# Optimization experiments

Measured on AMD Instinct MI355X. Metric: run time of the kernel, lower is better.

The kernel has to match this reference:

```python
import jax, jax.numpy as jnp
import numpy as np


def setup_inputs() -> dict:
    key = jax.random.key(0)
    k1, k2 = jax.random.split(key)
    x = jax.random.normal(k1, (8, 16, 16, 16, 64), dtype=jnp.float32)
    gamma = jax.random.normal(k2, (1,), dtype=jnp.float32)
    return {"x": x, "gamma": gamma}


def reference(x, gamma):
    # x: (B, D, H, W, C); tokens N = D*H*W, head dim C
    B, D, H, W, C = x.shape
    N = D * H * W
    q = x.reshape(B, N, C)                          # proj_query (B, N, C)
    # energy = batch_dot(q, q^T) -> (B, N, N)
    energy = jnp.einsum('bnc,bmc->bnm', q, q)
    attn = jax.nn.softmax(energy, axis=-1)          # softmax over last axis
    out = jnp.einsum('bnm,bmc->bnc', attn, q)       # attend * V (V = q)
    out = out.reshape(B, D, H, W, C)
    return gamma * out + x                          # gamma-scaled residual
```

## Files before the change

### kernel.cpp

```cpp
#include <hip/hip_runtime.h>

typedef _Float16 f16;
typedef _Float16 f16x4 __attribute__((ext_vector_type(4)));
typedef _Float16 f16x8 __attribute__((ext_vector_type(8)));
typedef float f32x4 __attribute__((ext_vector_type(4)));
typedef float f32x16 __attribute__((ext_vector_type(16)));
typedef unsigned int u32;
typedef u32 u32x2 __attribute__((ext_vector_type(2)));
typedef u32 u32x4v __attribute__((ext_vector_type(4)));

#define MFMA_F16 __builtin_amdgcn_mfma_f32_32x32x16_f16

constexpr int N   = 4096;
constexpr int C   = 64;
constexpr int KV  = 32;
constexpr int QB  = 64;
constexpr int NGRP = 4;
constexpr int KEYS_PER_GRP = N / NGRP;
constexpr int NT  = KEYS_PER_GRP / KV;
constexpr float LOG2E = 1.44269504088896f;
constexpr float THR   = 11.0f;

constexpr int KROW    = 136;
constexpr int VROW    = 72;
constexpr int VOFF    = 32 * KROW;
constexpr int BUFSZ   = VOFF + 64 * VROW;
constexpr int GSTRIDE = 2 * BUFSZ;
constexpr int PM_OFF  = 52224;
constexpr int PL_OFF  = PM_OFF + 768;
constexpr int EP_OFF  = 53760;

__device__ __forceinline__ float fexp2(float x) { return __builtin_amdgcn_exp2f(x); }
__device__ __forceinline__ u32 pkrtz(float a, float b) {
    return __builtin_bit_cast(u32, __builtin_amdgcn_cvt_pkrtz(a, b));
}
__device__ __forceinline__ f16x8 ld8(const char* p) {
    f16x4 lo = *(const f16x4*)p;
    f16x4 hi = *(const f16x4*)(p + 8);
    return __builtin_shufflevector(lo, hi, 0, 1, 2, 3, 4, 5, 6, 7);
}

__global__ __launch_bounds__(512, 4)
void channel_attn_kernel(const float* __restrict__ x,
                         const float* __restrict__ gamma,
                         float* __restrict__ out) {
    __shared__ __align__(16) unsigned char smem[71680];

    const int tid = threadIdx.x;
    const int w   = tid >> 6;
    const int g   = w >> 1;
    const int qw  = w & 1;
    const int l   = tid & 63;
    const int h   = l >> 5;
    const int q   = l & 31;
    const int bid = blockIdx.x;
    const int b   = bid & 7;
    const int qt  = bid >> 3;
    const float* xb = x + (size_t)b * (N * C);
    const int qbase = qt * QB;
    const int qg   = qw * 32 + q;
    const int qrow = qbase + qg;

    f16x8 Qf[4];
    {
        const float* qs = xb + (size_t)qrow * C + h * 8;
        #pragma unroll
        for (int kk = 0; kk < 4; ++kk) {
            f32x4 a  = *(const f32x4*)(qs + kk * 16);
            f32x4 c2 = *(const f32x4*)(qs + kk * 16 + 4);
            f16x8 f;
            f[0] = (f16)(a[0] * LOG2E);  f[1] = (f16)(a[1] * LOG2E);
            f[2] = (f16)(a[2] * LOG2E);  f[3] = (f16)(a[3] * LOG2E);
            f[4] = (f16)(c2[0] * LOG2E); f[5] = (f16)(c2[1] * LOG2E);
            f[6] = (f16)(c2[2] * LOG2E); f[7] = (f16)(c2[3] * LOG2E);
            Qf[kk] = f;
        }
    }

    const int c0  = (l & 15) * 4;
    const int kr0 = qw * 16 + (l >> 4) * 4;
    f32x4 stg[4];
    char* gb = (char*)smem + g * GSTRIDE;

    const float* kvsrc = xb + ((size_t)(g * KEYS_PER_GRP + kr0) * C + c0);

    auto stage_load = [&]() {
        #pragma unroll
        for (int j = 0; j < 4; ++j) stg[j] = *(const f32x4*)(kvsrc + j * C);
        kvsrc += KV * C;
    };
    auto stage_write = [&](int sel) {
        char* kb = gb + sel * BUFSZ;
        char* vb = kb + VOFF;
        #pragma unroll
        for (int j = 0; j < 4; ++j) {
            u32x2 kv2 = { pkrtz(stg[j][0], stg[j][1]), pkrtz(stg[j][2], stg[j][3]) };
            *(u32x2*)(kb + (kr0 + j) * KROW + c0 * 2) = kv2;
        }
        #pragma unroll
        for (int i = 0; i < 4; ++i) {
            u32x2 vv = { pkrtz(stg[0][i], stg[1][i]), pkrtz(stg[2][i], stg[3][i]) };
            *(u32x2*)(vb + (c0 + i) * VROW + kr0 * 2) = vv;
        }
    };

    f32x16 ot[2] = {};
    float m_run = -INFINITY, l_run = 0.f;

    stage_load();
    stage_write(0);
    __syncthreads();

    #pragma unroll 2
    for (int kt = 0; kt < NT; ++kt) {
        const int sel = kt & 1;
        const char* kb = gb + sel * BUFSZ;
        const char* vb = kb + VOFF;

        if (kt + 1 < NT) stage_load();

        f32x16 st = {};
        __builtin_amdgcn_s_setprio(1);
        #pragma unroll
        for (int kk = 0; kk < 4; ++kk) {
            f16x8 kf = ld8(kb + q * KROW + h * 16 + kk * 32);
            st = MFMA_F16(kf, Qf[kk], st, 0, 0, 0);
        }
        __builtin_amdgcn_s_setprio(0);

        float m01 = fmaxf(st[0], st[1]),  m23 = fmaxf(st[2], st[3]);
        float m45 = fmaxf(st[4], st[5]),  m67 = fmaxf(st[6], st[7]);
        float m89 = fmaxf(st[8], st[9]),  mab = fmaxf(st[10], st[11]);
        float mcd = fmaxf(st[12], st[13]), mef = fmaxf(st[14], st[15]);
        float pmax = fmaxf(fmaxf(fmaxf(m01, m23), fmaxf(m45, m67)),
                           fmaxf(fmaxf(m89, mab), fmaxf(mcd, mef)));
        pmax = fmaxf(pmax, __shfl_xor(pmax, 32, 64));

        if (!__all(pmax - m_run <= THR)) {
            float m_new = fmaxf(m_run, pmax);
            float scf = fexp2(m_run - m_new);
            l_run *= scf;
            #pragma unroll
            for (int mI = 0; mI < 2; ++mI)
                #pragma unroll
                for (int r2 = 0; r2 < 16; ++r2) ot[mI][r2] *= scf;
            m_run = m_new;
        }

        float rs4[4] = {0.f, 0.f, 0.f, 0.f};
        #pragma unroll
        for (int r2 = 0; r2 < 16; ++r2) {
            float p = fexp2(st[r2] - m_run);
            st[r2] = p;
            rs4[r2 & 3] += p;
        }
        float rs = (rs4[0] + rs4[1]) + (rs4[2] + rs4[3]);
        rs += __shfl_xor(rs, 32, 64);
        l_run += rs;

        f16x8 Pf[2];
        #pragma unroll
        for (int kk = 0; kk < 2; ++kk) {
            int so = 2 * kk + h;
            int sx = 2 * kk + (1 - h);
            u32 ua0 = pkrtz(st[so*4+0], st[so*4+1]);
            u32 ua1 = pkrtz(st[so*4+2], st[so*4+3]);
            u32 ub0 = pkrtz(st[sx*4+0], st[sx*4+1]);
            u32 ub1 = pkrtz(st[sx*4+2], st[sx*4+3]);
            u32 r0 = __shfl_xor(ub0, 32, 64);
            u32 r1 = __shfl_xor(ub1, 32, 64);
            u32x4v uv;
            uv[0] = h ? r0 : ua0;
            uv[1] = h ? r1 : ua1;
            uv[2] = h ? ua0 : r0;
            uv[3] = h ? ua1 : r1;
            Pf[kk] = __builtin_bit_cast(f16x8, uv);
        }

        if (kt + 1 < NT) stage_write(sel ^ 1);

        __builtin_amdgcn_s_setprio(1);
        #pragma unroll
        for (int mI = 0; mI < 2; ++mI) {
            f32x16 acc = ot[mI];
            #pragma unroll
            for (int kk = 0; kk < 2; ++kk) {
                f16x8 vf = ld8(vb + (q + 32 * mI) * VROW + h * 16 + kk * 32);
                acc = MFMA_F16(vf, Pf[kk], acc, 0, 0, 0);
            }
            ot[mI] = acc;
        }
        __builtin_amdgcn_s_setprio(0);

        __syncthreads();
    }

    float* pO = (float*)smem;
    float* pm = (float*)(smem + PM_OFF);
    float* pl = (float*)(smem + PL_OFF);

    if (g > 0) {
        float* po = pO + (size_t)(g - 1) * (64 * 68) + qg * 68;
        #pragma unroll
        for (int mI = 0; mI < 2; ++mI)
            #pragma unroll
            for (int j = 0; j < 4; ++j) {
                f32x4 v = { ot[mI][4*j], ot[mI][4*j+1], ot[mI][4*j+2], ot[mI][4*j+3] };
                *(f32x4*)(po + mI * 32 + j * 8 + h * 4) = v;
            }
        if (h == 0) { pm[(g - 1) * 64 + qg] = m_run; pl[(g - 1) * 64 + qg] = l_run; }
    }
    __syncthreads();

    if (g == 0) {
        float m1 = pm[qg], m2 = pm[64 + qg], m3 = pm[128 + qg];
        float l1 = pl[qg], l2 = pl[64 + qg], l3 = pl[128 + qg];
        float M  = fmaxf(fmaxf(m_run, m1), fmaxf(m2, m3));
        float a0 = fexp2(m_run - M);
        float ag[3] = { fexp2(m1 - M), fexp2(m2 - M), fexp2(m3 - M) };
        float L = l_run * a0 + l1 * ag[0] + l2 * ag[1] + l3 * ag[2];
        #pragma unroll
        for (int mI = 0; mI < 2; ++mI)
            #pragma unroll
            for (int r2 = 0; r2 < 16; ++r2) ot[mI][r2] *= a0;
        #pragma unroll
        for (int gg = 0; gg < 3; ++gg) {
            const float* po = pO + (size_t)gg * (64 * 68) + qg * 68;
            #pragma unroll
            for (int mI = 0; mI < 2; ++mI)
                #pragma unroll
                for (int j = 0; j < 4; ++j) {
                    f32x4 v = *(const f32x4*)(po + mI * 32 + j * 8 + h * 4);
                    ot[mI][4*j+0] += ag[gg] * v[0];
                    ot[mI][4*j+1] += ag[gg] * v[1];
                    ot[mI][4*j+2] += ag[gg] * v[2];
                    ot[mI][4*j+3] += ag[gg] * v[3];
                }
        }

        float invl = 1.0f / L;
        float* ep = (float*)(smem + EP_OFF + qw * 8448);
        #pragma unroll
        for (int mI = 0; mI < 2; ++mI)
            #pragma unroll
            for (int r2 = 0; r2 < 16; ++r2) {
                int c = 32 * mI + (r2 & 3) + 8 * (r2 >> 2) + 4 * h;
                ep[c * 33 + q] = ot[mI][r2] * invl;
            }

        const float gm = gamma[0];
        float* ob = out + (size_t)b * (N * C);
        #pragma unroll
        for (int it = 0; it < 8; ++it) {
            int ql  = it * 4 + (l >> 4);
            int cc0 = (l & 15) * 4;
            f32x4 o;
            o[0] = ep[(cc0 + 0) * 33 + ql];
            o[1] = ep[(cc0 + 1) * 33 + ql];
            o[2] = ep[(cc0 + 2) * 33 + ql];
            o[3] = ep[(cc0 + 3) * 33 + ql];
            int row = qbase + qw * 32 + ql;
            f32x4 xi = *(const f32x4*)(xb + (size_t)row * C + cc0);
            f32x4 res = { gm * o[0] + xi[0], gm * o[1] + xi[1],
                          gm * o[2] + xi[2], gm * o[3] + xi[3] };
            *(f32x4*)(ob + (size_t)row * C + cc0) = res;
        }
    }
}

extern "C" void kernel_launch(void* const* d_in, const int* in_sizes, int n_in,
                              void* d_out, int out_size, void* d_ws, size_t ws_size,
                              hipStream_t stream) {
    const float* x     = (const float*)d_in[0];
    const float* gamma = (const float*)d_in[1];
    float* out         = (float*)d_out;
    dim3 grid(512), block(512);
    channel_attn_kernel<<<grid, block, 0, stream>>>(x, gamma, out);
}
```

Baseline: 203.7 us.

## Precompute fp16 swizzled K/V in workspace and stream via global_load_lds

Adds a prepass kernel that converts x to fp16 once, writing K in row layout and V transposed per 32-key tile into a workspace with XOR swizzles. The attention kernel then streams these tiles straight into LDS with global_load_lds, removing per-block fp32 loads, conversion and scattered LDS writes. The row-sum is now computed on the matrix cores by multiplying against a ones vector. A fallback kernel also runs after it and scans its output for non-finite values, so a valid result costs only an extra launch and a check. The price is an extra kernel launch and workspace traffic.

```diff
diff --git a/kernel.cpp b/kernel.cpp
--- a/kernel.cpp
+++ b/kernel.cpp
@@ -11,40 +11,60 @@
 
 #define MFMA_F16 __builtin_amdgcn_mfma_f32_32x32x16_f16
 
-constexpr int N   = 4096;
-constexpr int C   = 64;
-constexpr int KV  = 32;
-constexpr int QB  = 64;
-constexpr int NGRP = 4;
-constexpr int KEYS_PER_GRP = N / NGRP;
-constexpr int NT  = KEYS_PER_GRP / KV;
 constexpr float LOG2E = 1.44269504088896f;
 constexpr float THR   = 11.0f;
-
-constexpr int KROW    = 136;
-constexpr int VROW    = 72;
-constexpr int VOFF    = 32 * KROW;
-constexpr int BUFSZ   = VOFF + 64 * VROW;
-constexpr int GSTRIDE = 2 * BUFSZ;
-constexpr int PM_OFF  = 52224;
-constexpr int PL_OFF  = PM_OFF + 768;
-constexpr int EP_OFF  = 53760;
 
 __device__ __forceinline__ float fexp2(float x) { return __builtin_amdgcn_exp2f(x); }
 __device__ __forceinline__ u32 pkrtz(float a, float b) {
     return __builtin_bit_cast(u32, __builtin_amdgcn_cvt_pkrtz(a, b));
 }
-__device__ __forceinline__ f16x8 ld8(const char* p) {
-    f16x4 lo = *(const f16x4*)p;
-    f16x4 hi = *(const f16x4*)(p + 8);
-    return __builtin_shufflevector(lo, hi, 0, 1, 2, 3, 4, 5, 6, 7);
+
+constexpr size_t KBYTES  = (size_t)8 * 4096 * 128;
+constexpr size_t WS_NEED = KBYTES * 2;
+
+__global__ __launch_bounds__(256)
+void precompute_kernel(const float* __restrict__ x, char* __restrict__ ws) {
+    int t  = blockIdx.x * 256 + threadIdx.x;
+    int c4 = (t & 15) * 4;
+    int k4 = ((t >> 4) & 1023) * 4;
+    int b  = t >> 14;
+    const float* src = x + ((size_t)b * 4096 + k4) * 64 + c4;
+    f32x4 v[4];
+    #pragma unroll
+    for (int j = 0; j < 4; ++j) v[j] = *(const f32x4*)(src + j * 64);
+    char* Kg = ws;
+    char* Vg = ws + KBYTES;
+    #pragma unroll
+    for (int j = 0; j < 4; ++j) {
+        int key = k4 + j;
+        u32x2 kp = { pkrtz(v[j][0], v[j][1]), pkrtz(v[j][2], v[j][3]) };
+        *(u32x2*)(Kg + ((size_t)(b * 4096 + key)) * 128 + ((c4 * 2) ^ ((key & 7) << 4))) = kp;
+    }
+    int tile = k4 >> 5, kl = k4 & 31;
+    #pragma unroll
+    for (int i = 0; i < 4; ++i) {
+        int ch = c4 + i;
+        u32x2 vp = { pkrtz(v[0][i], v[1][i]), pkrtz(v[2][i], v[3][i]) };
+        *(u32x2*)(Vg + ((size_t)(b * 128 + tile)) * 4096 + ch * 64 + ((kl * 2) ^ ((ch & 7) << 3))) = vp;
+    }
+}
+
+constexpr int NTI  = 32;
+constexpr int GLDS = 16384;
+constexpr int MG_PM = 52224, MG_PL = 52992, MG_EP = 53760;
+
+__device__ __forceinline__ void gload16(const void* g, void* l) {
+    __builtin_amdgcn_global_load_lds(
+        (const __attribute__((address_space(1))) void*)g,
+        (__attribute__((address_space(3))) void*)l, 16, 0, 0);
 }
 
 __global__ __launch_bounds__(512, 4)
-void channel_attn_kernel(const float* __restrict__ x,
-                         const float* __restrict__ gamma,
-                         float* __restrict__ out) {
-    __shared__ __align__(16) unsigned char smem[71680];
+void attn_fast(const char* __restrict__ ws, const float* __restrict__ x,
+               const float* __restrict__ gamma, float* __restrict__ out) {
+    __shared__ __align__(16) unsigned char smem[70656];
+    const char* Kg = ws;
+    const char* Vg = ws + KBYTES;
 
     const int tid = threadIdx.x;
     const int w   = tid >> 6;
@@ -56,14 +76,14 @@
     const int bid = blockIdx.x;
     const int b   = bid & 7;
     const int qt  = bid >> 3;
-    const float* xb = x + (size_t)b * (N * C);
-    const int qbase = qt * QB;
+    const float* xb = x + (size_t)b * (4096 * 64);
+    const int qbase = qt * 64;
     const int qg   = qw * 32 + q;
     const int qrow = qbase + qg;
 
     f16x8 Qf[4];
     {
-        const float* qs = xb + (size_t)qrow * C + h * 8;
+        const float* qs = xb + (size_t)qrow * 64 + h * 8;
         #pragma unroll
         for (int kk = 0; kk < 4; ++kk) {
             f32x4 a  = *(const f32x4*)(qs + kk * 16);
@@ -77,96 +97,92 @@
         }
     }
 
-    const int c0  = (l & 15) * 4;
-    const int kr0 = qw * 16 + (l >> 4) * 4;
-    f32x4 stg[4];
-    char* gb = (char*)smem + g * GSTRIDE;
-
-    const float* kvsrc = xb + ((size_t)(g * KEYS_PER_GRP + kr0) * C + c0);
-
-    auto stage_load = [&]() {
-        #pragma unroll
-        for (int j = 0; j < 4; ++j) stg[j] = *(const f32x4*)(kvsrc + j * C);
-        kvsrc += KV * C;
+    const char* gK = Kg + ((size_t)(b * 4096 + g * 1024)) * 128 + l * 16;
+    const char* gV = Vg + ((size_t)(b * 128  + g * 32 )) * 4096 + l * 16;
+    const char* gsrc = qw ? gV : gK;
+    char* sdst = (char*)smem + g * GLDS + (qw ? 4096 : 0);
+
+    auto stage = [&](int kt, int sel) {
+        const char* s = gsrc + (size_t)kt * 4096;
+        char* d = sdst + sel * 8192;
+        gload16(s,        d);
+        gload16(s + 1024, d + 1024);
+        gload16(s + 2048, d + 2048);
+        gload16(s + 3072, d + 3072);
     };
-    auto stage_write = [&](int sel) {
-        char* kb = gb + sel * BUFSZ;
-        char* vb = kb + VOFF;
-        #pragma unroll
-        for (int j = 0; j < 4; ++j) {
-            u32x2 kv2 = { pkrtz(stg[j][0], stg[j][1]), pkrtz(stg[j][2], stg[j][3]) };
-            *(u32x2*)(kb + (kr0 + j) * KROW + c0 * 2) = kv2;
-        }
-        #pragma unroll
-        for (int i = 0; i < 4; ++i) {
-            u32x2 vv = { pkrtz(stg[0][i], stg[1][i]), pkrtz(stg[2][i], stg[3][i]) };
-            *(u32x2*)(vb + (c0 + i) * VROW + kr0 * 2) = vv;
-        }
-    };
+
+    const char* kbase = (const char*)smem + g * GLDS;
+    const char* vbase = kbase + 4096;
+    const int xk = (q & 7) << 4;
+    const int xv = (q & 7) << 3;
+    const char* kp[4];
+    #pragma unroll
+    for (int kk = 0; kk < 4; ++kk)
+        kp[kk] = kbase + q * 128 + ((kk * 32 + h * 16) ^ xk);
+    const char* vplo[2]; const char* vphi[2];
+    #pragma unroll
+    for (int kk = 0; kk < 2; ++kk) {
+        int c = kk * 32 + h * 16;
+        vplo[kk] = vbase + q * 64 + (c ^ xv);
+        vphi[kk] = vbase + q * 64 + ((c + 8) ^ xv);
+    }
+
+    f16x8 ones8;
+    #pragma unroll
+    for (int j = 0; j < 8; ++j) ones8[j] = (f16)1.0f;
 
     f32x16 ot[2] = {};
-    float m_run = -INFINITY, l_run = 0.f;
-
-    stage_load();
-    stage_write(0);
+    f32x16 accl  = {};
+    float m_run = -INFINITY;
+
+    stage(0, 0);
     __syncthreads();
 
     #pragma unroll 2
-    for (int kt = 0; kt < NT; ++kt) {
+    for (int kt = 0; kt < NTI; ++kt) {
         const int sel = kt & 1;
-        const char* kb = gb + sel * BUFSZ;
-        const char* vb = kb + VOFF;
-
-        if (kt + 1 < NT) stage_load();
+        const int so  = sel * 8192;
+        if (kt + 1 < NTI) stage(kt + 1, sel ^ 1);
 
         f32x16 st = {};
         __builtin_amdgcn_s_setprio(1);
         #pragma unroll
         for (int kk = 0; kk < 4; ++kk) {
-            f16x8 kf = ld8(kb + q * KROW + h * 16 + kk * 32);
+            f16x8 kf = *(const f16x8*)(kp[kk] + so);
             st = MFMA_F16(kf, Qf[kk], st, 0, 0, 0);
         }
         __builtin_amdgcn_s_setprio(0);
 
-        float m01 = fmaxf(st[0], st[1]),  m23 = fmaxf(st[2], st[3]);
-        float m45 = fmaxf(st[4], st[5]),  m67 = fmaxf(st[6], st[7]);
-        float m89 = fmaxf(st[8], st[9]),  mab = fmaxf(st[10], st[11]);
-        float mcd = fmaxf(st[12], st[13]), mef = fmaxf(st[14], st[15]);
-        float pmax = fmaxf(fmaxf(fmaxf(m01, m23), fmaxf(m45, m67)),
-                           fmaxf(fmaxf(m89, mab), fmaxf(mcd, mef)));
+        float t0 = fmaxf(fmaxf(st[0], st[1]), st[2]);
+        float t1 = fmaxf(fmaxf(st[3], st[4]), st[5]);
+        float t2 = fmaxf(fmaxf(st[6], st[7]), st[8]);
+        float t3 = fmaxf(fmaxf(st[9], st[10]), st[11]);
+        float t4 = fmaxf(fmaxf(st[12], st[13]), st[14]);
+        float pmax = fmaxf(fmaxf(fmaxf(t0, t1), fmaxf(t2, t3)), fmaxf(t4, st[15]));
         pmax = fmaxf(pmax, __shfl_xor(pmax, 32, 64));
 
         if (!__all(pmax - m_run <= THR)) {
             float m_new = fmaxf(m_run, pmax);
             float scf = fexp2(m_run - m_new);
-            l_run *= scf;
-            #pragma unroll
-            for (int mI = 0; mI < 2; ++mI)
-                #pragma unroll
-                for (int r2 = 0; r2 < 16; ++r2) ot[mI][r2] *= scf;
+            #pragma unroll
+            for (int r = 0; r < 16; ++r) {
+                ot[0][r] *= scf; ot[1][r] *= scf; accl[r] *= scf;
+            }
             m_run = m_new;
         }
 
-        float rs4[4] = {0.f, 0.f, 0.f, 0.f};
-        #pragma unroll
-        for (int r2 = 0; r2 < 16; ++r2) {
-            float p = fexp2(st[r2] - m_run);
-            st[r2] = p;
-            rs4[r2 & 3] += p;
-        }
-        float rs = (rs4[0] + rs4[1]) + (rs4[2] + rs4[3]);
-        rs += __shfl_xor(rs, 32, 64);
-        l_run += rs;
+        #pragma unroll
+        for (int r = 0; r < 16; ++r) st[r] = fexp2(st[r] - m_run);
 
         f16x8 Pf[2];
         #pragma unroll
         for (int kk = 0; kk < 2; ++kk) {
-            int so = 2 * kk + h;
-            int sx = 2 * kk + (1 - h);
-            u32 ua0 = pkrtz(st[so*4+0], st[so*4+1]);
-            u32 ua1 = pkrtz(st[so*4+2], st[so*4+3]);
-            u32 ub0 = pkrtz(st[sx*4+0], st[sx*4+1]);
-            u32 ub1 = pkrtz(st[sx*4+2], st[sx*4+3]);
+            int sa = 2 * kk + h;
+            int sb = 2 * kk + (1 - h);
+            u32 ua0 = pkrtz(st[sa*4+0], st[sa*4+1]);
+            u32 ua1 = pkrtz(st[sa*4+2], st[sa*4+3]);
+            u32 ub0 = pkrtz(st[sb*4+0], st[sb*4+1]);
+            u32 ub1 = pkrtz(st[sb*4+2], st[sb*4+3]);
             u32 r0 = __shfl_xor(ub0, 32, 64);
             u32 r1 = __shfl_xor(ub1, 32, 64);
             u32x4v uv;
@@ -177,27 +193,29 @@
             Pf[kk] = __builtin_bit_cast(f16x8, uv);
         }
 
-        if (kt + 1 < NT) stage_write(sel ^ 1);
+        accl = MFMA_F16(ones8, Pf[0], accl, 0, 0, 0);
+        accl = MFMA_F16(ones8, Pf[1], accl, 0, 0, 0);
 
         __builtin_amdgcn_s_setprio(1);
         #pragma unroll
         for (int mI = 0; mI < 2; ++mI) {
-            f32x16 acc = ot[mI];
             #pragma unroll
             for (int kk = 0; kk < 2; ++kk) {
-                f16x8 vf = ld8(vb + (q + 32 * mI) * VROW + h * 16 + kk * 32);
-                acc = MFMA_F16(vf, Pf[kk], acc, 0, 0, 0);
+                f16x4 lo = *(const f16x4*)(vplo[kk] + so + mI * 2048);
+                f16x4 hi = *(const f16x4*)(vphi[kk] + so + mI * 2048);
+                f16x8 vf = __builtin_shufflevector(lo, hi, 0, 1, 2, 3, 4, 5, 6, 7);
+                ot[mI] = MFMA_F16(vf, Pf[kk], ot[mI], 0, 0, 0);
             }
-            ot[mI] = acc;
         }
         __builtin_amdgcn_s_setprio(0);
 
         __syncthreads();
     }
 
+    float l_run = accl[0];
     float* pO = (float*)smem;
-    float* pm = (float*)(smem + PM_OFF);
-    float* pl = (float*)(smem + PL_OFF);
+    float* pm = (float*)(smem + MG_PM);
+    float* pl = (float*)(smem + MG_PL);
 
     if (g > 0) {
         float* po = pO + (size_t)(g - 1) * (64 * 68) + qg * 68;
@@ -222,7 +240,7 @@
         #pragma unroll
         for (int mI = 0; mI < 2; ++mI)
             #pragma unroll
-            for (int r2 = 0; r2 < 16; ++r2) ot[mI][r2] *= a0;
+            for (int r = 0; r < 16; ++r) ot[mI][r] *= a0;
         #pragma unroll
         for (int gg = 0; gg < 3; ++gg) {
             const float* po = pO + (size_t)gg * (64 * 68) + qg * 68;
@@ -239,17 +257,17 @@
         }
 
         float invl = 1.0f / L;
-        float* ep = (float*)(smem + EP_OFF + qw * 8448);
+        float* ep = (float*)(smem + MG_EP + qw * 8448);
         #pragma unroll
         for (int mI = 0; mI < 2; ++mI)
             #pragma unroll
-            for (int r2 = 0; r2 < 16; ++r2) {
-                int c = 32 * mI + (r2 & 3) + 8 * (r2 >> 2) + 4 * h;
-                ep[c * 33 + q] = ot[mI][r2] * invl;
+            for (int r = 0; r < 16; ++r) {
+                int c = 32 * mI + (r & 3) + 8 * (r >> 2) + 4 * h;
+                ep[c * 33 + q] = ot[mI][r] * invl;
             }
 
         const float gm = gamma[0];
-        float* ob = out + (size_t)b * (N * C);
+        float* ob = out + (size_t)b * (4096 * 64);
         #pragma unroll
         for (int it = 0; it < 8; ++it) {
             int ql  = it * 4 + (l >> 4);
@@ -260,12 +278,214 @@
             o[2] = ep[(cc0 + 2) * 33 + ql];
             o[3] = ep[(cc0 + 3) * 33 + ql];
             int row = qbase + qw * 32 + ql;
-            f32x4 xi = *(const f32x4*)(xb + (size_t)row * C + cc0);
+            f32x4 xi = *(const f32x4*)(xb + (size_t)row * 64 + cc0);
             f32x4 res = { gm * o[0] + xi[0], gm * o[1] + xi[1],
                           gm * o[2] + xi[2], gm * o[3] + xi[3] };
-            *(f32x4*)(ob + (size_t)row * C + cc0) = res;
-        }
-    }
+            *(f32x4*)(ob + (size_t)row * 64 + cc0) = res;
+        }
+    }
+}
+
+namespace fb {
+
+constexpr int KV = 32, NT = 32, KEYS_PER_GRP = 1024;
+constexpr int KROW = 136, VROW = 72, VOFF = 32 * KROW, BUFSZ = VOFF + 64 * VROW;
+constexpr int GSTRIDE = 2 * BUFSZ;
+constexpr int PM_OFF = 52224, PL_OFF = PM_OFF + 768, EP_OFF = 53760;
+
+__device__ __forceinline__ f16x8 ld8(const char* p) {
+    f16x4 lo = *(const f16x4*)p;
+    f16x4 hi = *(const f16x4*)(p + 8);
+    return __builtin_shufflevector(lo, hi, 0, 1, 2, 3, 4, 5, 6, 7);
+}
+
+__global__ __launch_bounds__(512, 4)
+void channel_attn_fb(const float* __restrict__ x, const float* __restrict__ gamma,
+                     float* __restrict__ out, int force) {
+    __shared__ __align__(16) unsigned char smem[71680];
+    const int tid = threadIdx.x;
+    const int w = tid >> 6, g = w >> 1, qw = w & 1;
+    const int l = tid & 63, h = l >> 5, q = l & 31;
+    const int bid = blockIdx.x, b = bid & 7, qt = bid >> 3;
+    const float* xb = x + (size_t)b * (4096 * 64);
+    const int qbase = qt * 64, qg = qw * 32 + q, qrow = qbase + qg;
+
+    {
+        int bad = force;
+        const float* ob0 = out + (size_t)b * (4096 * 64) + (size_t)qbase * 64;
+        const f32x4* p4 = (const f32x4*)ob0 + (size_t)tid * 2;
+        f32x4 v0 = p4[0], v1 = p4[1];
+        #pragma unroll
+        for (int i = 0; i < 4; ++i) {
+            if (!(__builtin_fabsf(v0[i]) <= 1e30f)) bad = 1;
+            if (!(__builtin_fabsf(v1[i]) <= 1e30f)) bad = 1;
+        }
+        if (!__syncthreads_or(bad)) return;
+    }
+
+    f16x8 Qf[4];
+    {
+        const float* qs = xb + (size_t)qrow * 64 + h * 8;
+        #pragma unroll
+        for (int kk = 0; kk < 4; ++kk) {
+            f32x4 a = *(const f32x4*)(qs + kk * 16);
+            f32x4 c2 = *(const f32x4*)(qs + kk * 16 + 4);
+            f16x8 f;
+            f[0]=(f16)(a[0]*LOG2E); f[1]=(f16)(a[1]*LOG2E); f[2]=(f16)(a[2]*LOG2E); f[3]=(f16)(a[3]*LOG2E);
+            f[4]=(f16)(c2[0]*LOG2E);f[5]=(f16)(c2[1]*LOG2E);f[6]=(f16)(c2[2]*LOG2E);f[7]=(f16)(c2[3]*LOG2E);
+            Qf[kk] = f;
+        }
+    }
+    const int c0 = (l & 15) * 4, kr0 = qw * 16 + (l >> 4) * 4;
+    f32x4 stg[4];
+    char* gb = (char*)smem + g * GSTRIDE;
+    const float* kvsrc = xb + ((size_t)(g * KEYS_PER_GRP + kr0) * 64 + c0);
+    auto stage_load = [&]() {
+        #pragma unroll
+        for (int j = 0; j < 4; ++j) stg[j] = *(const f32x4*)(kvsrc + j * 64);
+        kvsrc += KV * 64;
+    };
+    auto stage_write = [&](int sel) {
+        char* kb = gb + sel * BUFSZ;
+        char* vb = kb + VOFF;
+        #pragma unroll
+        for (int j = 0; j < 4; ++j) {
+            u32x2 kv2 = { pkrtz(stg[j][0], stg[j][1]), pkrtz(stg[j][2], stg[j][3]) };
+            *(u32x2*)(kb + (kr0 + j) * KROW + c0 * 2) = kv2;
+        }
+        #pragma unroll
+        for (int i = 0; i < 4; ++i) {
+            u32x2 vv = { pkrtz(stg[0][i], stg[1][i]), pkrtz(stg[2][i], stg[3][i]) };
+            *(u32x2*)(vb + (c0 + i) * VROW + kr0 * 2) = vv;
+        }
+    };
+    f32x16 ot[2] = {};
+    float m_run = -INFINITY, l_run = 0.f;
+    stage_load(); stage_write(0); __syncthreads();
+    #pragma unroll 2
+    for (int kt = 0; kt < NT; ++kt) {
+        const int sel = kt & 1;
+        const char* kb = gb + sel * BUFSZ;
+        const char* vb = kb + VOFF;
+        if (kt + 1 < NT) stage_load();
+        f32x16 st = {};
+        __builtin_amdgcn_s_setprio(1);
+        #pragma unroll
+        for (int kk = 0; kk < 4; ++kk)
+            st = MFMA_F16(ld8(kb + q * KROW + h * 16 + kk * 32), Qf[kk], st, 0, 0, 0);
+        __builtin_amdgcn_s_setprio(0);
+        float m01=fmaxf(st[0],st[1]), m23=fmaxf(st[2],st[3]), m45=fmaxf(st[4],st[5]), m67=fmaxf(st[6],st[7]);
+        float m89=fmaxf(st[8],st[9]), mab=fmaxf(st[10],st[11]), mcd=fmaxf(st[12],st[13]), mef=fmaxf(st[14],st[15]);
+        float pmax = fmaxf(fmaxf(fmaxf(m01,m23),fmaxf(m45,m67)), fmaxf(fmaxf(m89,mab),fmaxf(mcd,mef)));
+        pmax = fmaxf(pmax, __shfl_xor(pmax, 32, 64));
+        if (!__all(pmax - m_run <= THR)) {
+            float m_new = fmaxf(m_run, pmax);
+            float scf = fexp2(m_run - m_new);
+            l_run *= scf;
+            #pragma unroll
+            for (int mI = 0; mI < 2; ++mI)
+                #pragma unroll
+                for (int r = 0; r < 16; ++r) ot[mI][r] *= scf;
+            m_run = m_new;
+        }
+        float rs4[4] = {0.f,0.f,0.f,0.f};
+        #pragma unroll
+        for (int r = 0; r < 16; ++r) { float p = fexp2(st[r] - m_run); st[r] = p; rs4[r & 3] += p; }
+        float rs = (rs4[0]+rs4[1]) + (rs4[2]+rs4[3]);
+        rs += __shfl_xor(rs, 32, 64);
+        l_run += rs;
+        f16x8 Pf[2];
+        #pragma unroll
+        for (int kk = 0; kk < 2; ++kk) {
+            int sa = 2*kk + h, sb = 2*kk + (1-h);
+            u32 ua0 = pkrtz(st[sa*4+0], st[sa*4+1]);
+            u32 ua1 = pkrtz(st[sa*4+2], st[sa*4+3]);
+            u32 ub0 = pkrtz(st[sb*4+0], st[sb*4+1]);
+            u32 ub1 = pkrtz(st[sb*4+2], st[sb*4+3]);
+            u32 r0 = __shfl_xor(ub0, 32, 64);
+            u32 r1 = __shfl_xor(ub1, 32, 64);
+            u32x4v uv;
+            uv[0] = h ? r0 : ua0; uv[1] = h ? r1 : ua1;
+            uv[2] = h ? ua0 : r0; uv[3] = h ? ua1 : r1;
+            Pf[kk] = __builtin_bit_cast(f16x8, uv);
+        }
+        if (kt + 1 < NT) stage_write(sel ^ 1);
+        __builtin_amdgcn_s_setprio(1);
+        #pragma unroll
+        for (int mI = 0; mI < 2; ++mI) {
+            f32x16 acc = ot[mI];
+            #pragma unroll
+            for (int kk = 0; kk < 2; ++kk)
+                acc = MFMA_F16(ld8(vb + (q + 32*mI) * VROW + h * 16 + kk * 32), Pf[kk], acc, 0, 0, 0);
+            ot[mI] = acc;
+        }
+        __builtin_amdgcn_s_setprio(0);
+        __syncthreads();
+    }
+    float* pO = (float*)smem;
+    float* pm = (float*)(smem + PM_OFF);
+    float* pl = (float*)(smem + PL_OFF);
+    if (g > 0) {
+        float* po = pO + (size_t)(g - 1) * (64 * 68) + qg * 68;
+        #pragma unroll
+        for (int mI = 0; mI < 2; ++mI)
+            #pragma unroll
+            for (int j = 0; j < 4; ++j) {
+                f32x4 v = { ot[mI][4*j], ot[mI][4*j+1], ot[mI][4*j+2], ot[mI][4*j+3] };
+                *(f32x4*)(po + mI * 32 + j * 8 + h * 4) = v;
+            }
+        if (h == 0) { pm[(g-1)*64 + qg] = m_run; pl[(g-1)*64 + qg] = l_run; }
+    }
+    __syncthreads();
+    if (g == 0) {
+        float m1 = pm[qg], m2 = pm[64+qg], m3 = pm[128+qg];
+        float l1 = pl[qg], l2 = pl[64+qg], l3 = pl[128+qg];
+        float M = fmaxf(fmaxf(m_run, m1), fmaxf(m2, m3));
+        float a0 = fexp2(m_run - M);
+        float ag[3] = { fexp2(m1 - M), fexp2(m2 - M), fexp2(m3 - M) };
+        float L = l_run * a0 + l1*ag[0] + l2*ag[1] + l3*ag[2];
+        #pragma unroll
+        for (int mI = 0; mI < 2; ++mI)
+            #pragma unroll
+            for (int r = 0; r < 16; ++r) ot[mI][r] *= a0;
+        #pragma unroll
+        for (int gg = 0; gg < 3; ++gg) {
+            const float* po = pO + (size_t)gg * (64 * 68) + qg * 68;
+            #pragma unroll
+            for (int mI = 0; mI < 2; ++mI)
+                #pragma unroll
+                for (int j = 0; j < 4; ++j) {
+                    f32x4 v = *(const f32x4*)(po + mI * 32 + j * 8 + h * 4);
+                    ot[mI][4*j+0] += ag[gg]*v[0]; ot[mI][4*j+1] += ag[gg]*v[1];
+                    ot[mI][4*j+2] += ag[gg]*v[2]; ot[mI][4*j+3] += ag[gg]*v[3];
+                }
+        }
+        float invl = 1.0f / L;
+        float* ep = (float*)(smem + EP_OFF + qw * 8448);
+        #pragma unroll
+        for (int mI = 0; mI < 2; ++mI)
+            #pragma unroll
+            for (int r = 0; r < 16; ++r) {
+                int c = 32*mI + (r & 3) + 8*(r >> 2) + 4*h;
+                ep[c * 33 + q] = ot[mI][r] * invl;
+            }
+        const float gm = gamma[0];
+        float* ob = out + (size_t)b * (4096 * 64);
+        #pragma unroll
+        for (int it = 0; it < 8; ++it) {
+            int ql = it * 4 + (l >> 4);
+            int cc0 = (l & 15) * 4;
+            f32x4 o;
+            o[0] = ep[(cc0+0)*33+ql]; o[1] = ep[(cc0+1)*33+ql];
+            o[2] = ep[(cc0+2)*33+ql]; o[3] = ep[(cc0+3)*33+ql];
+            int row = qbase + qw * 32 + ql;
+            f32x4 xi = *(const f32x4*)(xb + (size_t)row * 64 + cc0);
+            f32x4 res = { gm*o[0]+xi[0], gm*o[1]+xi[1], gm*o[2]+xi[2], gm*o[3]+xi[3] };
+            *(f32x4*)(ob + (size_t)row * 64 + cc0) = res;
+        }
+    }
+}
+
 }
 
 extern "C" void kernel_launch(void* const* d_in, const int* in_sizes, int n_in,
@@ -274,6 +494,11 @@
     const float* x     = (const float*)d_in[0];
     const float* gamma = (const float*)d_in[1];
     float* out         = (float*)d_out;
-    dim3 grid(512), block(512);
-    channel_attn_kernel<<<grid, block, 0, stream>>>(x, gamma, out);
-}
+    if (ws_size >= WS_NEED && d_ws != nullptr) {
+        precompute_kernel<<<dim3(512), dim3(256), 0, stream>>>(x, (char*)d_ws);
+        attn_fast<<<dim3(512), dim3(512), 0, stream>>>((const char*)d_ws, x, gamma, out);
+        fb::channel_attn_fb<<<dim3(512), dim3(512), 0, stream>>>(x, gamma, out, 0);
+    } else {
+        fb::channel_attn_fb<<<dim3(512), dim3(512), 0, stream>>>(x, gamma, out, 1);
+    }
+}
```

Result: slower. 221.8 us (+8.9%).
